# Kernel optimization log

Measured on AMD Instinct MI355X. Metric: run time of the kernel, lower is better.

The kernel has to match this reference:

```python
import jax, jax.numpy as jnp
import numpy as np

NUM_EMBEDDINGS = 1024
EMBEDDING_DIM = 64
COMMITMENT_COST = 0.25


def setup_inputs() -> dict:
    key = jax.random.key(0)
    kz, kc = jax.random.split(key)
    z = jax.random.normal(kz, (16, 2048, EMBEDDING_DIM), dtype=jnp.float32)
    # nn.Embedding weight init: uniform(-1/K, 1/K)
    codebook = (jax.random.uniform(kc, (NUM_EMBEDDINGS, EMBEDDING_DIM), dtype=jnp.float32) * 2.0 - 1.0) / NUM_EMBEDDINGS
    return {"z": z, "codebook": codebook}


def reference(z, codebook):
    D = codebook.shape[1]
    K = codebook.shape[0]
    flat_z = z.reshape(-1, D)  # [N, D]
    # squared L2 distances: ||z||^2 + ||e||^2 - 2 z.e  -> [N, K]
    distances = (
        jnp.sum(flat_z ** 2, axis=1, keepdims=True)
        + jnp.sum(codebook ** 2, axis=1)
        - 2.0 * jnp.matmul(flat_z, codebook.T)
    )
    encoding_indices = jnp.argmin(distances, axis=1)  # [N]
    quantized = codebook[encoding_indices].reshape(z.shape)

    e_latent_loss = jnp.mean((jax.lax.stop_gradient(quantized) - z) ** 2)
    q_latent_loss = jnp.mean((quantized - jax.lax.stop_gradient(z)) ** 2)
    vq_loss = q_latent_loss + COMMITMENT_COST * e_latent_loss

    # straight-through estimator
    quantized_st = z + jax.lax.stop_gradient(quantized - z)

    # perplexity from codebook usage histogram
    n = encoding_indices.shape[0]
    counts = jnp.zeros((K,), dtype=jnp.float32).at[encoding_indices].add(1.0)
    avg_probs = counts / n
    perplexity = jnp.exp(-jnp.sum(avg_probs * jnp.log(avg_probs + 1e-10)))

    indices_out = encoding_indices.reshape(z.shape[:-1])
    return quantized_st, vq_loss, indices_out, perplexity
```

## Files before the change

### kernel.cpp

```cpp
#include <hip/hip_runtime.h>
#include <math.h>


#define D 64
#define KC 1024
#define ROWS 64
#define TC 32
#define NT (KC / TC)
#define NP (NT / 2)
#define BCH 33
#define TILE_SH (16 * BCH * 8)

typedef short short8 __attribute__((ext_vector_type(8)));
typedef short short4v __attribute__((ext_vector_type(4)));
typedef float f32x4 __attribute__((ext_vector_type(4)));

__device__ __forceinline__ unsigned short f2bf(float x) {
  unsigned int u = __float_as_uint(x);
  unsigned int r = (u + 0x7fffu + ((u >> 16) & 1u)) >> 16;
  return (unsigned short)r;
}
__device__ __forceinline__ float bf2f(unsigned short h) {
  return __uint_as_float((unsigned int)h << 16);
}

__device__ __forceinline__ void split8(const float4 a, const float4 b,
                                       short8* hi, short8* lo) {
  float f[8] = {a.x, a.y, a.z, a.w, b.x, b.y, b.z, b.w};
#pragma unroll
  for (int i = 0; i < 8; ++i) {
    unsigned short h = f2bf(f[i]);
    (*hi)[i] = (short)h;
    (*lo)[i] = (short)f2bf(f[i] - bf2f(h));
  }
}

__global__ __launch_bounds__(256) void vq_prep(
    const float* __restrict__ cb, unsigned short* __restrict__ bsplit,
    float* __restrict__ cbn, unsigned int* __restrict__ hist,
    float* __restrict__ loss_acc) {
  const int k = blockIdx.x * 256 + threadIdx.x;
  const float4* e = (const float4*)(cb + (size_t)k * D);
  unsigned short* bp = bsplit + (size_t)k * 128;
  float s0 = 0.f, s1 = 0.f, s2 = 0.f, s3 = 0.f;
#pragma unroll
  for (int i = 0; i < 16; ++i) {
    float4 v = e[i];
    s0 = fmaf(v.x, v.x, s0);
    s1 = fmaf(v.y, v.y, s1);
    s2 = fmaf(v.z, v.z, s2);
    s3 = fmaf(v.w, v.w, s3);
    unsigned short h0 = f2bf(v.x), h1 = f2bf(v.y), h2 = f2bf(v.z), h3 = f2bf(v.w);
    short4v hv = {(short)h0, (short)h1, (short)h2, (short)h3};
    short4v lv = {(short)f2bf(v.x - bf2f(h0)), (short)f2bf(v.y - bf2f(h1)),
                  (short)f2bf(v.z - bf2f(h2)), (short)f2bf(v.w - bf2f(h3))};
    *(short4v*)(bp + i * 4) = hv;
    *(short4v*)(bp + 64 + i * 4) = lv;
  }
  cbn[k] = (s0 + s1) + (s2 + s3);
  hist[k] = 0u;
  if (k == 0) loss_acc[0] = 0.f;
}

__global__ __launch_bounds__(256, 3) void vq_main(
    const float* __restrict__ z, const unsigned short* __restrict__ bsplit,
    const float* __restrict__ cbn, const float* __restrict__ cb,
    float* __restrict__ out_q, float* __restrict__ out_idx,
    unsigned int* __restrict__ hist, float* __restrict__ loss_acc) {
  __shared__ __align__(16) unsigned short Bsh[2][2][TILE_SH];
  __shared__ float scbn[KC];
  __shared__ int skf[ROWS];
  __shared__ float swav[4];
  __shared__ unsigned int lhist[KC];

  const int tid = threadIdx.x;
  const int lane = tid & 63;
  const int wav = tid >> 6;
  const int quad = lane >> 4;
  const int col = lane & 15;
  const int rowbase = blockIdx.x * ROWS;

  const int arow = rowbase + wav * 16 + col;
  const float4* zr = (const float4*)(z + (size_t)arow * D);
  const float4 f0 = zr[quad * 2];
  const float4 f1 = zr[quad * 2 + 1];
  const float4 f2 = zr[8 + quad * 2];
  const float4 f3 = zr[8 + quad * 2 + 1];

  *(float4*)&scbn[tid * 4] = *(const float4*)&cbn[tid * 4];
#pragma unroll
  for (int j = 0; j < KC / 256; ++j) lhist[tid + 256 * j] = 0u;

  const int cslot = (tid & 15) * BCH + (tid >> 4);
#pragma unroll
  for (int T = 0; T < 2; ++T) {
    const size_t off =
        (size_t)(T * TC + (tid >> 4)) * 128 + (size_t)(tid & 15) * 8;
    short8 s0 = *(const short8*)(bsplit + off);
    short8 s1 = *(const short8*)(bsplit + off + 2048);
    *(short8*)&Bsh[0][T][cslot * 8] = s0;
    *(short8*)&Bsh[0][T][(cslot + 16) * 8] = s1;
  }

  short8 a0, a1, a2, a3;
  split8(f0, f1, &a0, &a2);
  split8(f2, f3, &a1, &a3);

  float nrm = ((f0.x * f0.x + f0.y * f0.y) + (f0.z * f0.z + f0.w * f0.w)) +
              ((f1.x * f1.x + f1.y * f1.y) + (f1.z * f1.z + f1.w * f1.w)) +
              ((f2.x * f2.x + f2.y * f2.y) + (f2.z * f2.z + f2.w * f2.w)) +
              ((f3.x * f3.x + f3.y * f3.y) + (f3.z * f3.z + f3.w * f3.w));
  nrm += __shfl_xor(nrm, 16, 64);
  nrm += __shfl_xor(nrm, 32, 64);
  float rzv[4];
#pragma unroll
  for (int r = 0; r < 4; ++r) rzv[r] = __shfl(nrm, quad * 4 + r, 64);

  __syncthreads();

  float b1d[4], b2d[4];
  int b1k[4], b2k[4];
#pragma unroll
  for (int i = 0; i < 4; ++i) {
    b1d[i] = 3.4e38f; b2d[i] = 3.4e38f;
    b1k[i] = 0x7fffffff; b2k[i] = 0x7fffffff;
  }

  for (int p = 0; p < NP; ++p) {
    short8 st00, st01, st10, st11;
    if (p + 1 < NP) {
      const size_t base = (size_t)((p + 1) * 2) * TC;
      const size_t o0 = (base + (tid >> 4)) * 128 + (size_t)(tid & 15) * 8;
      st00 = *(const short8*)(bsplit + o0);
      st01 = *(const short8*)(bsplit + o0 + 2048);
      st10 = *(const short8*)(bsplit + o0 + 4096);
      st11 = *(const short8*)(bsplit + o0 + 6144);
    }
#pragma unroll
    for (int T = 0; T < 2; ++T) {
      const int kb = (p * 2 + T) * TC;
      const unsigned short* bcur = &Bsh[p & 1][T][0];
      const float enA = scbn[kb + col];
      const float enB = scbn[kb + 16 + col];
      const short8 bA0 = *(const short8*)(bcur + ((0 + quad) * BCH + col) * 8);
      const short8 bA1 = *(const short8*)(bcur + ((4 + quad) * BCH + col) * 8);
      const short8 bA2 = *(const short8*)(bcur + ((8 + quad) * BCH + col) * 8);
      const short8 bA3 = *(const short8*)(bcur + ((12 + quad) * BCH + col) * 8);
      const short8 bB0 =
          *(const short8*)(bcur + ((0 + quad) * BCH + col + 16) * 8);
      const short8 bB1 =
          *(const short8*)(bcur + ((4 + quad) * BCH + col + 16) * 8);
      const short8 bB2 =
          *(const short8*)(bcur + ((8 + quad) * BCH + col + 16) * 8);
      const short8 bB3 =
          *(const short8*)(bcur + ((12 + quad) * BCH + col + 16) * 8);

      f32x4 accA = {0.f, 0.f, 0.f, 0.f}, accB = {0.f, 0.f, 0.f, 0.f};
      accA = __builtin_amdgcn_mfma_f32_16x16x32_bf16(a0, bA0, accA, 0, 0, 0);
      accB = __builtin_amdgcn_mfma_f32_16x16x32_bf16(a0, bB0, accB, 0, 0, 0);
      accA = __builtin_amdgcn_mfma_f32_16x16x32_bf16(a1, bA1, accA, 0, 0, 0);
      accB = __builtin_amdgcn_mfma_f32_16x16x32_bf16(a1, bB1, accB, 0, 0, 0);
      accA = __builtin_amdgcn_mfma_f32_16x16x32_bf16(a2, bA0, accA, 0, 0, 0);
      accB = __builtin_amdgcn_mfma_f32_16x16x32_bf16(a2, bB0, accB, 0, 0, 0);
      accA = __builtin_amdgcn_mfma_f32_16x16x32_bf16(a3, bA1, accA, 0, 0, 0);
      accB = __builtin_amdgcn_mfma_f32_16x16x32_bf16(a3, bB1, accB, 0, 0, 0);
      accA = __builtin_amdgcn_mfma_f32_16x16x32_bf16(a0, bA2, accA, 0, 0, 0);
      accB = __builtin_amdgcn_mfma_f32_16x16x32_bf16(a0, bB2, accB, 0, 0, 0);
      accA = __builtin_amdgcn_mfma_f32_16x16x32_bf16(a1, bA3, accA, 0, 0, 0);
      accB = __builtin_amdgcn_mfma_f32_16x16x32_bf16(a1, bB3, accB, 0, 0, 0);

#pragma unroll
      for (int reg = 0; reg < 4; ++reg) {
        {
          float d = fmaf(-2.0f, accA[reg], rzv[reg] + enA);
          int k = kb + col;
          bool w1 = d < b1d[reg];
          bool w2 = d < b2d[reg];
          b2d[reg] = w1 ? b1d[reg] : (w2 ? d : b2d[reg]);
          b2k[reg] = w1 ? b1k[reg] : (w2 ? k : b2k[reg]);
          b1d[reg] = w1 ? d : b1d[reg];
          b1k[reg] = w1 ? k : b1k[reg];
        }
        {
          float d = fmaf(-2.0f, accB[reg], rzv[reg] + enB);
          int k = kb + 16 + col;
          bool w1 = d < b1d[reg];
          bool w2 = d < b2d[reg];
          b2d[reg] = w1 ? b1d[reg] : (w2 ? d : b2d[reg]);
          b2k[reg] = w1 ? b1k[reg] : (w2 ? k : b2k[reg]);
          b1d[reg] = w1 ? d : b1d[reg];
          b1k[reg] = w1 ? k : b1k[reg];
        }
      }
    }

    if (p + 1 < NP) {
      unsigned short* bn0 = &Bsh[(p + 1) & 1][0][0];
      unsigned short* bn1 = &Bsh[(p + 1) & 1][1][0];
      *(short8*)&bn0[cslot * 8] = st00;
      *(short8*)&bn0[(cslot + 16) * 8] = st01;
      *(short8*)&bn1[cslot * 8] = st10;
      *(short8*)&bn1[(cslot + 16) * 8] = st11;
    }
    __syncthreads();
  }

#pragma unroll
  for (int m = 1; m < 16; m <<= 1) {
#pragma unroll
    for (int reg = 0; reg < 4; ++reg) {
      float od1 = __shfl_xor(b1d[reg], m, 64);
      int ok1 = __shfl_xor(b1k[reg], m, 64);
      float od2 = __shfl_xor(b2d[reg], m, 64);
      int ok2 = __shfl_xor(b2k[reg], m, 64);
      bool fo = (od1 < b1d[reg]) || (od1 == b1d[reg] && ok1 < b1k[reg]);
      float w1 = fo ? od1 : b1d[reg];
      int wk1 = fo ? ok1 : b1k[reg];
      float l1 = fo ? b1d[reg] : od1;
      int lk1 = fo ? b1k[reg] : ok1;
      bool so = (od2 < b2d[reg]) || (od2 == b2d[reg] && ok2 < b2k[reg]);
      float m2 = so ? od2 : b2d[reg];
      int mk2 = so ? ok2 : b2k[reg];
      bool lw = (l1 < m2) || (l1 == m2 && lk1 < mk2);
      b1d[reg] = w1;
      b1k[reg] = wk1;
      b2d[reg] = lw ? l1 : m2;
      b2k[reg] = lw ? lk1 : mk2;
    }
  }

  if (col < 4) {
    const int row = wav * 16 + quad * 4 + col;
    float bd1 = b1d[col], bd2 = b2d[col];
    int bk1 = b1k[col], bk2 = b2k[col];
    if (bd2 - bd1 < 1e-5f) {
      const int grow = rowbase + row;
      const float4* zp = (const float4*)(z + (size_t)grow * D);
      float s0 = 0.f, s1 = 0.f, s2 = 0.f, s3 = 0.f;
#pragma unroll
      for (int i = 0; i < 16; ++i) {
        float4 v = zp[i];
        s0 = fmaf(v.x, v.x, s0);
        s1 = fmaf(v.y, v.y, s1);
        s2 = fmaf(v.z, v.z, s2);
        s3 = fmaf(v.w, v.w, s3);
      }
      const float rzx = (s0 + s1) + (s2 + s3);
      float dx[2];
      int kk[2] = {bk1, bk2};
#pragma unroll
      for (int c = 0; c < 2; ++c) {
        const float4* e4 = (const float4*)(cb + (size_t)kk[c] * D);
        float d0 = 0.f, d1 = 0.f, d2 = 0.f, d3 = 0.f;
#pragma unroll
        for (int i = 0; i < 16; ++i) {
          float4 v = e4[i];
          float4 zv = zp[i];
          d0 = fmaf(zv.x, v.x, d0);
          d1 = fmaf(zv.y, v.y, d1);
          d2 = fmaf(zv.z, v.z, d2);
          d3 = fmaf(zv.w, v.w, d3);
        }
        float dot = (d0 + d1) + (d2 + d3);
        dx[c] = (rzx + scbn[kk[c]]) - 2.0f * dot;
      }
      if ((dx[1] < dx[0]) || (dx[1] == dx[0] && bk2 < bk1)) bk1 = bk2;
    }
    skf[row] = bk1;
    out_idx[rowbase + row] = (float)bk1;
    atomicAdd(&lhist[bk1], 1u);
  }
  __syncthreads();

#pragma unroll
  for (int j = 0; j < KC / 256; ++j) {
    unsigned int c = lhist[tid + 256 * j];
    if (c) atomicAdd(&hist[tid + 256 * j], c);
  }

  float lsum = 0.f;
#pragma unroll
  for (int it = 0; it < 4; ++it) {
    int f4 = it * 256 + tid;
    int r = f4 >> 4;
    int c4 = (f4 & 15) * 4;
    int bk = skf[r];
    const float4 q = *(const float4*)(cb + (size_t)bk * D + c4);
    const int grow = rowbase + r;
    const float4 zv = *(const float4*)(z + (size_t)grow * D + c4);
    *(float4*)(out_q + (size_t)grow * D + c4) = q;
    float ax = q.x - zv.x, ay = q.y - zv.y, az = q.z - zv.z, aw = q.w - zv.w;
    lsum += ax * ax + ay * ay + az * az + aw * aw;
  }
#pragma unroll
  for (int off = 32; off > 0; off >>= 1) lsum += __shfl_down(lsum, off, 64);
  if (lane == 0) swav[wav] = lsum;
  __syncthreads();
  if (tid == 0) {
    atomicAdd(loss_acc, (swav[0] + swav[1]) + (swav[2] + swav[3]));
  }
}

__global__ __launch_bounds__(1024) void vq_final(
    const unsigned int* __restrict__ hist, const float* __restrict__ loss_acc,
    float* __restrict__ out_loss, float* __restrict__ out_perp, float inv_n,
    float inv_nd) {
  __shared__ float part[16];
  const int t = threadIdx.x;
  const int lane = t & 63;
  const int wav = t >> 6;
  float p = (float)hist[t] * inv_n;
  float v = p * logf(p + 1e-10f);
#pragma unroll
  for (int off = 32; off > 0; off >>= 1) v += __shfl_down(v, off, 64);
  if (lane == 0) part[wav] = v;
  __syncthreads();
  if (t == 0) {
    float s = 0.f;
#pragma unroll
    for (int j = 0; j < 16; ++j) s += part[j];
    *out_perp = expf(-s);
    *out_loss = 1.25f * loss_acc[0] * inv_nd;
  }
}

extern "C" void kernel_launch(void* const* d_in, const int* in_sizes, int n_in,
                              void* d_out, int out_size, void* d_ws,
                              size_t ws_size, hipStream_t stream) {
  (void)n_in;
  (void)out_size;
  (void)ws_size;
  const float* z = (const float*)d_in[0];
  const float* cb = (const float*)d_in[1];
  const int N = in_sizes[0] / D;

  float* out_q = (float*)d_out;
  float* out_loss = (float*)d_out + (size_t)N * D;
  float* out_idx = out_loss + 1;
  float* out_perp = out_idx + N;

  unsigned int* hist = (unsigned int*)d_ws;
  float* loss_acc = (float*)d_ws + 1024;
  float* cbn = (float*)d_ws + 1040;
  unsigned short* bsplit = (unsigned short*)((float*)d_ws + 2064);

  vq_prep<<<dim3(KC / 256), dim3(256), 0, stream>>>(cb, bsplit, cbn, hist,
                                                    loss_acc);
  vq_main<<<dim3(N / ROWS), dim3(256), 0, stream>>>(z, bsplit, cbn, cb, out_q,
                                                    out_idx, hist, loss_acc);
  vq_final<<<dim3(1), dim3(1024), 0, stream>>>(
      hist, loss_acc, out_loss, out_perp, 1.0f / (float)N,
      1.0f / ((float)N * (float)D));
}
```

Baseline: 97.67 us.

## Load codebook fragments directly from global into registers, drop LDS staging

Replaces the LDS double-buffered codebook tile staging and per-iteration __syncthreads with direct per-lane global (L2-cached) loads of the bf16 B fragments, software-pipelined across two register sets. Launch bounds drop from 3 to 2 blocks per CU to make room for the extra registers. This removes LDS writes, reads and barriers, but every wave now fetches the codebook itself through the cache, which adds global traffic and load latency and may lower occupancy.

```diff
diff --git a/kernel.cpp b/kernel.cpp
--- a/kernel.cpp
+++ b/kernel.cpp
@@ -7,9 +7,6 @@
 #define ROWS 64
 #define TC 32
 #define NT (KC / TC)
-#define NP (NT / 2)
-#define BCH 33
-#define TILE_SH (16 * BCH * 8)
 
 typedef short short8 __attribute__((ext_vector_type(8)));
 typedef short short4v __attribute__((ext_vector_type(4)));
@@ -62,12 +59,11 @@
   if (k == 0) loss_acc[0] = 0.f;
 }
 
-__global__ __launch_bounds__(256, 3) void vq_main(
+__global__ __launch_bounds__(256, 2) void vq_main(
     const float* __restrict__ z, const unsigned short* __restrict__ bsplit,
     const float* __restrict__ cbn, const float* __restrict__ cb,
     float* __restrict__ out_q, float* __restrict__ out_idx,
     unsigned int* __restrict__ hist, float* __restrict__ loss_acc) {
-  __shared__ __align__(16) unsigned short Bsh[2][2][TILE_SH];
   __shared__ float scbn[KC];
   __shared__ int skf[ROWS];
   __shared__ float swav[4];
@@ -91,16 +87,8 @@
 #pragma unroll
   for (int j = 0; j < KC / 256; ++j) lhist[tid + 256 * j] = 0u;
 
-  const int cslot = (tid & 15) * BCH + (tid >> 4);
-#pragma unroll
-  for (int T = 0; T < 2; ++T) {
-    const size_t off =
-        (size_t)(T * TC + (tid >> 4)) * 128 + (size_t)(tid & 15) * 8;
-    short8 s0 = *(const short8*)(bsplit + off);
-    short8 s1 = *(const short8*)(bsplit + off + 2048);
-    *(short8*)&Bsh[0][T][cslot * 8] = s0;
-    *(short8*)&Bsh[0][T][(cslot + 16) * 8] = s1;
-  }
+  const unsigned short* pbA = bsplit + (size_t)col * 128 + quad * 8;
+  const unsigned short* pbB = pbA + 16 * 128;
 
   short8 a0, a1, a2, a3;
   split8(f0, f1, &a0, &a2);
@@ -126,83 +114,76 @@
     b1k[i] = 0x7fffffff; b2k[i] = 0x7fffffff;
   }
 
-  for (int p = 0; p < NP; ++p) {
-    short8 st00, st01, st10, st11;
-    if (p + 1 < NP) {
-      const size_t base = (size_t)((p + 1) * 2) * TC;
-      const size_t o0 = (base + (tid >> 4)) * 128 + (size_t)(tid & 15) * 8;
-      st00 = *(const short8*)(bsplit + o0);
-      st01 = *(const short8*)(bsplit + o0 + 2048);
-      st10 = *(const short8*)(bsplit + o0 + 4096);
-      st11 = *(const short8*)(bsplit + o0 + 6144);
-    }
-#pragma unroll
-    for (int T = 0; T < 2; ++T) {
-      const int kb = (p * 2 + T) * TC;
-      const unsigned short* bcur = &Bsh[p & 1][T][0];
-      const float enA = scbn[kb + col];
-      const float enB = scbn[kb + 16 + col];
-      const short8 bA0 = *(const short8*)(bcur + ((0 + quad) * BCH + col) * 8);
-      const short8 bA1 = *(const short8*)(bcur + ((4 + quad) * BCH + col) * 8);
-      const short8 bA2 = *(const short8*)(bcur + ((8 + quad) * BCH + col) * 8);
-      const short8 bA3 = *(const short8*)(bcur + ((12 + quad) * BCH + col) * 8);
-      const short8 bB0 =
-          *(const short8*)(bcur + ((0 + quad) * BCH + col + 16) * 8);
-      const short8 bB1 =
-          *(const short8*)(bcur + ((4 + quad) * BCH + col + 16) * 8);
-      const short8 bB2 =
-          *(const short8*)(bcur + ((8 + quad) * BCH + col + 16) * 8);
-      const short8 bB3 =
-          *(const short8*)(bcur + ((12 + quad) * BCH + col + 16) * 8);
-
-      f32x4 accA = {0.f, 0.f, 0.f, 0.f}, accB = {0.f, 0.f, 0.f, 0.f};
-      accA = __builtin_amdgcn_mfma_f32_16x16x32_bf16(a0, bA0, accA, 0, 0, 0);
-      accB = __builtin_amdgcn_mfma_f32_16x16x32_bf16(a0, bB0, accB, 0, 0, 0);
-      accA = __builtin_amdgcn_mfma_f32_16x16x32_bf16(a1, bA1, accA, 0, 0, 0);
-      accB = __builtin_amdgcn_mfma_f32_16x16x32_bf16(a1, bB1, accB, 0, 0, 0);
-      accA = __builtin_amdgcn_mfma_f32_16x16x32_bf16(a2, bA0, accA, 0, 0, 0);
-      accB = __builtin_amdgcn_mfma_f32_16x16x32_bf16(a2, bB0, accB, 0, 0, 0);
-      accA = __builtin_amdgcn_mfma_f32_16x16x32_bf16(a3, bA1, accA, 0, 0, 0);
-      accB = __builtin_amdgcn_mfma_f32_16x16x32_bf16(a3, bB1, accB, 0, 0, 0);
-      accA = __builtin_amdgcn_mfma_f32_16x16x32_bf16(a0, bA2, accA, 0, 0, 0);
-      accB = __builtin_amdgcn_mfma_f32_16x16x32_bf16(a0, bB2, accB, 0, 0, 0);
-      accA = __builtin_amdgcn_mfma_f32_16x16x32_bf16(a1, bA3, accA, 0, 0, 0);
-      accB = __builtin_amdgcn_mfma_f32_16x16x32_bf16(a1, bB3, accB, 0, 0, 0);
-
-#pragma unroll
-      for (int reg = 0; reg < 4; ++reg) {
-        {
-          float d = fmaf(-2.0f, accA[reg], rzv[reg] + enA);
-          int k = kb + col;
-          bool w1 = d < b1d[reg];
-          bool w2 = d < b2d[reg];
-          b2d[reg] = w1 ? b1d[reg] : (w2 ? d : b2d[reg]);
-          b2k[reg] = w1 ? b1k[reg] : (w2 ? k : b2k[reg]);
-          b1d[reg] = w1 ? d : b1d[reg];
-          b1k[reg] = w1 ? k : b1k[reg];
-        }
-        {
-          float d = fmaf(-2.0f, accB[reg], rzv[reg] + enB);
-          int k = kb + 16 + col;
-          bool w1 = d < b1d[reg];
-          bool w2 = d < b2d[reg];
-          b2d[reg] = w1 ? b1d[reg] : (w2 ? d : b2d[reg]);
-          b2k[reg] = w1 ? b1k[reg] : (w2 ? k : b2k[reg]);
-          b1d[reg] = w1 ? d : b1d[reg];
-          b1k[reg] = w1 ? k : b1k[reg];
-        }
+  auto load_tile = [&](int kb, short8& bA0, short8& bA1, short8& bA2,
+                       short8& bA3, short8& bB0, short8& bB1, short8& bB2,
+                       short8& bB3) {
+    const unsigned short* pA = pbA + (size_t)kb * 128;
+    const unsigned short* pB = pbB + (size_t)kb * 128;
+    bA0 = *(const short8*)(pA + 0);
+    bA1 = *(const short8*)(pA + 32);
+    bA2 = *(const short8*)(pA + 64);
+    bA3 = *(const short8*)(pA + 96);
+    bB0 = *(const short8*)(pB + 0);
+    bB1 = *(const short8*)(pB + 32);
+    bB2 = *(const short8*)(pB + 64);
+    bB3 = *(const short8*)(pB + 96);
+  };
+
+  auto compute_tile = [&](int kb, const short8 bA0, const short8 bA1,
+                          const short8 bA2, const short8 bA3, const short8 bB0,
+                          const short8 bB1, const short8 bB2,
+                          const short8 bB3) {
+    const float enA = scbn[kb + col];
+    const float enB = scbn[kb + 16 + col];
+    f32x4 accA = {0.f, 0.f, 0.f, 0.f}, accB = {0.f, 0.f, 0.f, 0.f};
+    accA = __builtin_amdgcn_mfma_f32_16x16x32_bf16(a0, bA0, accA, 0, 0, 0);
+    accB = __builtin_amdgcn_mfma_f32_16x16x32_bf16(a0, bB0, accB, 0, 0, 0);
+    accA = __builtin_amdgcn_mfma_f32_16x16x32_bf16(a1, bA1, accA, 0, 0, 0);
+    accB = __builtin_amdgcn_mfma_f32_16x16x32_bf16(a1, bB1, accB, 0, 0, 0);
+    accA = __builtin_amdgcn_mfma_f32_16x16x32_bf16(a2, bA0, accA, 0, 0, 0);
+    accB = __builtin_amdgcn_mfma_f32_16x16x32_bf16(a2, bB0, accB, 0, 0, 0);
+    accA = __builtin_amdgcn_mfma_f32_16x16x32_bf16(a3, bA1, accA, 0, 0, 0);
+    accB = __builtin_amdgcn_mfma_f32_16x16x32_bf16(a3, bB1, accB, 0, 0, 0);
+    accA = __builtin_amdgcn_mfma_f32_16x16x32_bf16(a0, bA2, accA, 0, 0, 0);
+    accB = __builtin_amdgcn_mfma_f32_16x16x32_bf16(a0, bB2, accB, 0, 0, 0);
+    accA = __builtin_amdgcn_mfma_f32_16x16x32_bf16(a1, bA3, accA, 0, 0, 0);
+    accB = __builtin_amdgcn_mfma_f32_16x16x32_bf16(a1, bB3, accB, 0, 0, 0);
+
+#pragma unroll
+    for (int reg = 0; reg < 4; ++reg) {
+      {
+        float d = fmaf(-2.0f, accA[reg], rzv[reg] + enA);
+        int k = kb + col;
+        bool w1 = d < b1d[reg];
+        bool w2 = d < b2d[reg];
+        b2d[reg] = w1 ? b1d[reg] : (w2 ? d : b2d[reg]);
+        b2k[reg] = w1 ? b1k[reg] : (w2 ? k : b2k[reg]);
+        b1d[reg] = w1 ? d : b1d[reg];
+        b1k[reg] = w1 ? k : b1k[reg];
+      }
+      {
+        float d = fmaf(-2.0f, accB[reg], rzv[reg] + enB);
+        int k = kb + 16 + col;
+        bool w1 = d < b1d[reg];
+        bool w2 = d < b2d[reg];
+        b2d[reg] = w1 ? b1d[reg] : (w2 ? d : b2d[reg]);
+        b2k[reg] = w1 ? b1k[reg] : (w2 ? k : b2k[reg]);
+        b1d[reg] = w1 ? d : b1d[reg];
+        b1k[reg] = w1 ? k : b1k[reg];
       }
     }
-
-    if (p + 1 < NP) {
-      unsigned short* bn0 = &Bsh[(p + 1) & 1][0][0];
-      unsigned short* bn1 = &Bsh[(p + 1) & 1][1][0];
-      *(short8*)&bn0[cslot * 8] = st00;
-      *(short8*)&bn0[(cslot + 16) * 8] = st01;
-      *(short8*)&bn1[cslot * 8] = st10;
-      *(short8*)&bn1[(cslot + 16) * 8] = st11;
+  };
+
+  short8 xA0, xA1, xA2, xA3, xB0, xB1, xB2, xB3;
+  short8 yA0, yA1, yA2, yA3, yB0, yB1, yB2, yB3;
+  load_tile(0, xA0, xA1, xA2, xA3, xB0, xB1, xB2, xB3);
+  for (int t = 0; t < NT; t += 2) {
+    load_tile((t + 1) * TC, yA0, yA1, yA2, yA3, yB0, yB1, yB2, yB3);
+    compute_tile(t * TC, xA0, xA1, xA2, xA3, xB0, xB1, xB2, xB3);
+    if (t + 2 < NT) {
+      load_tile((t + 2) * TC, xA0, xA1, xA2, xA3, xB0, xB1, xB2, xB3);
     }
-    __syncthreads();
+    compute_tile((t + 1) * TC, yA0, yA1, yA2, yA3, yB0, yB1, yB2, yB3);
   }
 
 #pragma unroll
```

Measured after the change: 133.3 us. 36.5% more time.

## Stage four codebook tiles per barrier and split top-2 tracking into two chains

Applied to the files above, without the earlier changes.

Each pipeline stage now loads and stages four 32-code tiles into LDS instead of two, which halves the number of __syncthreads iterations. The top-2 running argmin is split into two independent accumulator sets, one for the first two tiles and one for the last two, to shorten the serial compare/select dependency chain; the sets are merged before the cross-lane reduction. This doubles LDS use for the B tiles, adds registers for the prefetch and accumulators, and lowers the launch-bounds occupancy hint from 3 to 2 blocks per CU, which may reduce latency hiding.

```diff
diff --git a/kernel.cpp b/kernel.cpp
--- a/kernel.cpp
+++ b/kernel.cpp
@@ -7,7 +7,7 @@
 #define ROWS 64
 #define TC 32
 #define NT (KC / TC)
-#define NP (NT / 2)
+#define NQ (NT / 4)
 #define BCH 33
 #define TILE_SH (16 * BCH * 8)
 
@@ -62,12 +62,12 @@
   if (k == 0) loss_acc[0] = 0.f;
 }
 
-__global__ __launch_bounds__(256, 3) void vq_main(
+__global__ __launch_bounds__(256, 2) void vq_main(
     const float* __restrict__ z, const unsigned short* __restrict__ bsplit,
     const float* __restrict__ cbn, const float* __restrict__ cb,
     float* __restrict__ out_q, float* __restrict__ out_idx,
     unsigned int* __restrict__ hist, float* __restrict__ loss_acc) {
-  __shared__ __align__(16) unsigned short Bsh[2][2][TILE_SH];
+  __shared__ __align__(16) unsigned short Bsh[2][4][TILE_SH];
   __shared__ float scbn[KC];
   __shared__ int skf[ROWS];
   __shared__ float swav[4];
@@ -93,13 +93,13 @@
 
   const int cslot = (tid & 15) * BCH + (tid >> 4);
 #pragma unroll
-  for (int T = 0; T < 2; ++T) {
+  for (int T = 0; T < 4; ++T) {
     const size_t off =
         (size_t)(T * TC + (tid >> 4)) * 128 + (size_t)(tid & 15) * 8;
-    short8 s0 = *(const short8*)(bsplit + off);
-    short8 s1 = *(const short8*)(bsplit + off + 2048);
-    *(short8*)&Bsh[0][T][cslot * 8] = s0;
-    *(short8*)&Bsh[0][T][(cslot + 16) * 8] = s1;
+    short8 q0 = *(const short8*)(bsplit + off);
+    short8 q1 = *(const short8*)(bsplit + off + 2048);
+    *(short8*)&Bsh[0][T][cslot * 8] = q0;
+    *(short8*)&Bsh[0][T][(cslot + 16) * 8] = q1;
   }
 
   short8 a0, a1, a2, a3;
@@ -118,27 +118,43 @@
 
   __syncthreads();
 
-  float b1d[4], b2d[4];
-  int b1k[4], b2k[4];
+  float b1dA[4], b2dA[4], b1dB[4], b2dB[4];
+  int b1kA[4], b2kA[4], b1kB[4], b2kB[4];
 #pragma unroll
   for (int i = 0; i < 4; ++i) {
-    b1d[i] = 3.4e38f; b2d[i] = 3.4e38f;
-    b1k[i] = 0x7fffffff; b2k[i] = 0x7fffffff;
-  }
-
-  for (int p = 0; p < NP; ++p) {
-    short8 st00, st01, st10, st11;
-    if (p + 1 < NP) {
-      const size_t base = (size_t)((p + 1) * 2) * TC;
+    b1dA[i] = 3.4e38f; b2dA[i] = 3.4e38f;
+    b1kA[i] = 0x7fffffff; b2kA[i] = 0x7fffffff;
+    b1dB[i] = 3.4e38f; b2dB[i] = 3.4e38f;
+    b1kB[i] = 0x7fffffff; b2kB[i] = 0x7fffffff;
+  }
+
+  auto fold = [&](float (&B1D)[4], int (&B1K)[4], float (&B2D)[4],
+                  int (&B2K)[4], float d, int k, int reg) {
+    bool w1 = d < B1D[reg];
+    bool w2 = d < B2D[reg];
+    B2D[reg] = w1 ? B1D[reg] : (w2 ? d : B2D[reg]);
+    B2K[reg] = w1 ? B1K[reg] : (w2 ? k : B2K[reg]);
+    B1D[reg] = w1 ? d : B1D[reg];
+    B1K[reg] = w1 ? k : B1K[reg];
+  };
+
+  for (int p = 0; p < NQ; ++p) {
+    short8 s0, s1, s2, s3, s4, s5, s6, s7;
+    if (p + 1 < NQ) {
+      const size_t base = (size_t)((p + 1) * 4) * TC;
       const size_t o0 = (base + (tid >> 4)) * 128 + (size_t)(tid & 15) * 8;
-      st00 = *(const short8*)(bsplit + o0);
-      st01 = *(const short8*)(bsplit + o0 + 2048);
-      st10 = *(const short8*)(bsplit + o0 + 4096);
-      st11 = *(const short8*)(bsplit + o0 + 6144);
-    }
-#pragma unroll
-    for (int T = 0; T < 2; ++T) {
-      const int kb = (p * 2 + T) * TC;
+      s0 = *(const short8*)(bsplit + o0);
+      s1 = *(const short8*)(bsplit + o0 + 2048);
+      s2 = *(const short8*)(bsplit + o0 + 4096);
+      s3 = *(const short8*)(bsplit + o0 + 6144);
+      s4 = *(const short8*)(bsplit + o0 + 8192);
+      s5 = *(const short8*)(bsplit + o0 + 10240);
+      s6 = *(const short8*)(bsplit + o0 + 12288);
+      s7 = *(const short8*)(bsplit + o0 + 14336);
+    }
+#pragma unroll
+    for (int T = 0; T < 4; ++T) {
+      const int kb = (p * 4 + T) * TC;
       const unsigned short* bcur = &Bsh[p & 1][T][0];
       const float enA = scbn[kb + col];
       const float enB = scbn[kb + 16 + col];
@@ -171,68 +187,86 @@
 
 #pragma unroll
       for (int reg = 0; reg < 4; ++reg) {
-        {
-          float d = fmaf(-2.0f, accA[reg], rzv[reg] + enA);
-          int k = kb + col;
-          bool w1 = d < b1d[reg];
-          bool w2 = d < b2d[reg];
-          b2d[reg] = w1 ? b1d[reg] : (w2 ? d : b2d[reg]);
-          b2k[reg] = w1 ? b1k[reg] : (w2 ? k : b2k[reg]);
-          b1d[reg] = w1 ? d : b1d[reg];
-          b1k[reg] = w1 ? k : b1k[reg];
-        }
-        {
-          float d = fmaf(-2.0f, accB[reg], rzv[reg] + enB);
-          int k = kb + 16 + col;
-          bool w1 = d < b1d[reg];
-          bool w2 = d < b2d[reg];
-          b2d[reg] = w1 ? b1d[reg] : (w2 ? d : b2d[reg]);
-          b2k[reg] = w1 ? b1k[reg] : (w2 ? k : b2k[reg]);
-          b1d[reg] = w1 ? d : b1d[reg];
-          b1k[reg] = w1 ? k : b1k[reg];
+        if (T < 2) {
+          fold(b1dA, b1kA, b2dA, b2kA, fmaf(-2.0f, accA[reg], rzv[reg] + enA),
+               kb + col, reg);
+          fold(b1dA, b1kA, b2dA, b2kA, fmaf(-2.0f, accB[reg], rzv[reg] + enB),
+               kb + 16 + col, reg);
+        } else {
+          fold(b1dB, b1kB, b2dB, b2kB, fmaf(-2.0f, accA[reg], rzv[reg] + enA),
+               kb + col, reg);
+          fold(b1dB, b1kB, b2dB, b2kB, fmaf(-2.0f, accB[reg], rzv[reg] + enB),
+               kb + 16 + col, reg);
         }
       }
     }
 
-    if (p + 1 < NP) {
+    if (p + 1 < NQ) {
       unsigned short* bn0 = &Bsh[(p + 1) & 1][0][0];
       unsigned short* bn1 = &Bsh[(p + 1) & 1][1][0];
-      *(short8*)&bn0[cslot * 8] = st00;
-      *(short8*)&bn0[(cslot + 16) * 8] = st01;
-      *(short8*)&bn1[cslot * 8] = st10;
-      *(short8*)&bn1[(cslot + 16) * 8] = st11;
+      unsigned short* bn2 = &Bsh[(p + 1) & 1][2][0];
+      unsigned short* bn3 = &Bsh[(p + 1) & 1][3][0];
+      *(short8*)&bn0[cslot * 8] = s0;
+      *(short8*)&bn0[(cslot + 16) * 8] = s1;
+      *(short8*)&bn1[cslot * 8] = s2;
+      *(short8*)&bn1[(cslot + 16) * 8] = s3;
+      *(short8*)&bn2[cslot * 8] = s4;
+      *(short8*)&bn2[(cslot + 16) * 8] = s5;
+      *(short8*)&bn3[cslot * 8] = s6;
+      *(short8*)&bn3[(cslot + 16) * 8] = s7;
     }
     __syncthreads();
   }
 
 #pragma unroll
+  for (int reg = 0; reg < 4; ++reg) {
+    float od1 = b1dB[reg];
+    int ok1 = b1kB[reg];
+    float od2 = b2dB[reg];
+    int ok2 = b2kB[reg];
+    bool fo = (od1 < b1dA[reg]) || (od1 == b1dA[reg] && ok1 < b1kA[reg]);
+    float w1 = fo ? od1 : b1dA[reg];
+    int wk1 = fo ? ok1 : b1kA[reg];
+    float l1 = fo ? b1dA[reg] : od1;
+    int lk1 = fo ? b1kA[reg] : ok1;
+    bool so = (od2 < b2dA[reg]) || (od2 == b2dA[reg] && ok2 < b2kA[reg]);
+    float m2 = so ? od2 : b2dA[reg];
+    int mk2 = so ? ok2 : b2kA[reg];
+    bool lw = (l1 < m2) || (l1 == m2 && lk1 < mk2);
+    b1dA[reg] = w1;
+    b1kA[reg] = wk1;
+    b2dA[reg] = lw ? l1 : m2;
+    b2kA[reg] = lw ? lk1 : mk2;
+  }
+
+#pragma unroll
   for (int m = 1; m < 16; m <<= 1) {
 #pragma unroll
     for (int reg = 0; reg < 4; ++reg) {
-      float od1 = __shfl_xor(b1d[reg], m, 64);
-      int ok1 = __shfl_xor(b1k[reg], m, 64);
-      float od2 = __shfl_xor(b2d[reg], m, 64);
-      int ok2 = __shfl_xor(b2k[reg], m, 64);
-      bool fo = (od1 < b1d[reg]) || (od1 == b1d[reg] && ok1 < b1k[reg]);
-      float w1 = fo ? od1 : b1d[reg];
-      int wk1 = fo ? ok1 : b1k[reg];
-      float l1 = fo ? b1d[reg] : od1;
-      int lk1 = fo ? b1k[reg] : ok1;
-      bool so = (od2 < b2d[reg]) || (od2 == b2d[reg] && ok2 < b2k[reg]);
-      float m2 = so ? od2 : b2d[reg];
-      int mk2 = so ? ok2 : b2k[reg];
+      float od1 = __shfl_xor(b1dA[reg], m, 64);
+      int ok1 = __shfl_xor(b1kA[reg], m, 64);
+      float od2 = __shfl_xor(b2dA[reg], m, 64);
+      int ok2 = __shfl_xor(b2kA[reg], m, 64);
+      bool fo = (od1 < b1dA[reg]) || (od1 == b1dA[reg] && ok1 < b1kA[reg]);
+      float w1 = fo ? od1 : b1dA[reg];
+      int wk1 = fo ? ok1 : b1kA[reg];
+      float l1 = fo ? b1dA[reg] : od1;
+      int lk1 = fo ? b1kA[reg] : ok1;
+      bool so = (od2 < b2dA[reg]) || (od2 == b2dA[reg] && ok2 < b2kA[reg]);
+      float m2 = so ? od2 : b2dA[reg];
+      int mk2 = so ? ok2 : b2kA[reg];
       bool lw = (l1 < m2) || (l1 == m2 && lk1 < mk2);
-      b1d[reg] = w1;
-      b1k[reg] = wk1;
-      b2d[reg] = lw ? l1 : m2;
-      b2k[reg] = lw ? lk1 : mk2;
+      b1dA[reg] = w1;
+      b1kA[reg] = wk1;
+      b2dA[reg] = lw ? l1 : m2;
+      b2kA[reg] = lw ? lk1 : mk2;
     }
   }
 
   if (col < 4) {
     const int row = wav * 16 + quad * 4 + col;
-    float bd1 = b1d[col], bd2 = b2d[col];
-    int bk1 = b1k[col], bk2 = b2k[col];
+    float bd1 = b1dA[col], bd2 = b2dA[col];
+    int bk1 = b1kA[col], bk2 = b2kA[col];
     if (bd2 - bd1 < 1e-5f) {
       const int grow = rowbase + row;
       const float4* zp = (const float4*)(z + (size_t)grow * D);
```

Result: no change. 98.88 us (+1.2%).
